# Kernel optimization log

Hardware: AMD Instinct MI355X
Metric: run time of the kernel (lower is better)

## Reference

```python
import jax, jax.numpy as jnp
import numpy as np

N_NODES = 2_000_000
N_EDGES = 16_777_216
N_REL = 4


def setup_inputs() -> dict:
    key = jax.random.key(0)
    ks = jax.random.split(key, 13)
    inp = {
        "author_x": jax.random.normal(ks[0], (N_NODES, 4), jnp.float32),
        "paper_x": jax.random.normal(ks[1], (N_NODES, 4), jnp.float32),
        "src_index": jax.random.randint(ks[2], (N_EDGES,), 0, N_NODES, jnp.int64 if jax.config.jax_enable_x64 else jnp.int32).astype(jnp.int32),
        "dst_index": jax.random.randint(ks[3], (N_EDGES,), 0, N_NODES).astype(jnp.int32),
        "edge_type_index": jax.random.randint(ks[4], (N_EDGES,), 0, N_REL).astype(jnp.int32),
        "edge_src_is_paper": jax.random.randint(ks[5], (N_REL,), 0, 2).astype(jnp.int32),
        "edge_dst_is_paper": jax.random.randint(ks[6], (N_REL,), 0, 2).astype(jnp.int32),
        "Wa": jax.random.normal(ks[7], (4, 4), jnp.float32) * 0.5,
        "ba": jax.random.normal(ks[8], (4,), jnp.float32) * 0.1,
        "Wp": jax.random.normal(ks[9], (4, 4), jnp.float32) * 0.5,
        "bp": jax.random.normal(ks[10], (4,), jnp.float32) * 0.1,
        "Ws": jax.random.normal(ks[11], (8,), jnp.float32) * 0.5,
        "bs": jax.random.normal(ks[12], (1,), jnp.float32) * 0.1,
    }
    return inp


def reference(author_x, paper_x, src_index, dst_index, edge_type_index,
              edge_src_is_paper, edge_dst_is_paper, Wa, ba, Wp, bp, Ws, bs):
    # Encode node tables (tiny GEMMs): [N,4] @ [4,4]^T + [4]
    author_h = author_x @ Wa.T + ba
    paper_h = paper_x @ Wp.T + bp
    # Per-edge relation-type dispatch: 1 = paper table, 0 = author table
    src_p = edge_src_is_paper[edge_type_index].astype(bool)  # [E]
    dst_p = edge_dst_is_paper[edge_type_index].astype(bool)  # [E]
    src_repr = jnp.where(src_p[:, None], paper_h[src_index], author_h[src_index])  # [E,4]
    dst_repr = jnp.where(dst_p[:, None], paper_h[dst_index], author_h[dst_index])  # [E,4]
    # scorer: Linear(8,1) on concat, squeeze last dim -> [E]
    logits = jnp.concatenate([src_repr, dst_repr], axis=-1) @ Ws + bs[0]
    return logits
```

## Files before the change

### kernel.cpp

```cpp
#include <hip/hip_runtime.h>

typedef int         iv4 __attribute__((ext_vector_type(4)));
typedef float       fv4 __attribute__((ext_vector_type(4)));
typedef _Float16    hv4 __attribute__((ext_vector_type(4)));

struct Fold {
    float va_s[4], va_d[4], vp_s[4], vp_d[4];
    float ca_s, ca_d, cp_s, cp_d;
};

__device__ inline Fold make_fold(const float* __restrict__ Wa, const float* __restrict__ ba,
                                 const float* __restrict__ Wp, const float* __restrict__ bp,
                                 const float* __restrict__ Ws) {
    Fold f;
    float w0 = Ws[0], w1 = Ws[1], w2 = Ws[2], w3 = Ws[3];
    float w4 = Ws[4], w5 = Ws[5], w6 = Ws[6], w7 = Ws[7];
#pragma unroll
    for (int j = 0; j < 4; ++j) {
        f.va_s[j] = w0*Wa[j] + w1*Wa[4+j] + w2*Wa[8+j] + w3*Wa[12+j];
        f.va_d[j] = w4*Wa[j] + w5*Wa[4+j] + w6*Wa[8+j] + w7*Wa[12+j];
        f.vp_s[j] = w0*Wp[j] + w1*Wp[4+j] + w2*Wp[8+j] + w3*Wp[12+j];
        f.vp_d[j] = w4*Wp[j] + w5*Wp[4+j] + w6*Wp[8+j] + w7*Wp[12+j];
    }
    f.ca_s = w0*ba[0] + w1*ba[1] + w2*ba[2] + w3*ba[3];
    f.ca_d = w4*ba[0] + w5*ba[1] + w6*ba[2] + w7*ba[3];
    f.cp_s = w0*bp[0] + w1*bp[1] + w2*bp[2] + w3*bp[3];
    f.cp_d = w4*bp[0] + w5*bp[1] + w6*bp[2] + w7*bp[3];
    return f;
}

__device__ inline void node_scores(const Fold& f, fv4 a, fv4 p,
                                   float& as, float& ps, float& ad, float& pd) {
    as = a.x*f.va_s[0] + a.y*f.va_s[1] + a.z*f.va_s[2] + a.w*f.va_s[3] + f.ca_s;
    ad = a.x*f.va_d[0] + a.y*f.va_d[1] + a.z*f.va_d[2] + a.w*f.va_d[3] + f.ca_d;
    ps = p.x*f.vp_s[0] + p.y*f.vp_s[1] + p.z*f.vp_s[2] + p.w*f.vp_s[3] + f.cp_s;
    pd = p.x*f.vp_d[0] + p.y*f.vp_d[1] + p.z*f.vp_d[2] + p.w*f.vp_d[3] + f.cp_d;
}

__global__ __launch_bounds__(256) void node_pass1(
    const fv4* __restrict__ ax, const fv4* __restrict__ px,
    const float* __restrict__ Wa, const float* __restrict__ ba,
    const float* __restrict__ Wp, const float* __restrict__ bp,
    const float* __restrict__ Ws,
    hv4* __restrict__ sc, unsigned* __restrict__ maxes, int n,
    const iv4* __restrict__ et4, unsigned* __restrict__ et8w, int n_et4)
{
    Fold f = make_fold(Wa, ba, Wp, bp, Ws);
    float ms = 0.f, md = 0.f;
    int stride = gridDim.x * blockDim.x;
    int tid0 = blockIdx.x * blockDim.x + threadIdx.x;
    for (int i = tid0; i < n; i += stride) {
        fv4 a = __builtin_nontemporal_load(ax + i);
        fv4 p = __builtin_nontemporal_load(px + i);
        float as, ps, ad, pd;
        node_scores(f, a, p, as, ps, ad, pd);
        hv4 h;
        h.x = (_Float16)as; h.y = (_Float16)ps; h.z = (_Float16)ad; h.w = (_Float16)pd;
        __builtin_nontemporal_store(h, sc + i);
        ms = fmaxf(ms, fmaxf(fabsf(as), fabsf(ps)));
        md = fmaxf(md, fmaxf(fabsf(ad), fabsf(pd)));
    }
    if (et8w) {
        for (int j = tid0; j < n_et4; j += stride) {
            iv4 t = __builtin_nontemporal_load(et4 + j);
            unsigned b = (unsigned)(t.x & 3) | ((unsigned)(t.y & 3) << 8)
                       | ((unsigned)(t.z & 3) << 16) | ((unsigned)(t.w & 3) << 24);
            __builtin_nontemporal_store(b, et8w + j);
        }
    }
#pragma unroll
    for (int off = 32; off >= 1; off >>= 1) {
        ms = fmaxf(ms, __shfl_down(ms, off));
        md = fmaxf(md, __shfl_down(md, off));
    }
    __shared__ float lms[4], lmd[4];
    int wave = threadIdx.x >> 6, lane = threadIdx.x & 63;
    if (lane == 0) { lms[wave] = ms; lmd[wave] = md; }
    __syncthreads();
    if (threadIdx.x == 0) {
        float bms = fmaxf(fmaxf(lms[0], lms[1]), fmaxf(lms[2], lms[3]));
        float bmd = fmaxf(fmaxf(lmd[0], lmd[1]), fmaxf(lmd[2], lmd[3]));
        atomicMax(&maxes[0], __float_as_uint(bms));
        atomicMax(&maxes[1], __float_as_uint(bmd));
    }
}

__global__ __launch_bounds__(256) void node_pass2(
    const hv4* __restrict__ sc, const unsigned* __restrict__ maxes,
    signed char* __restrict__ ts, signed char* __restrict__ td, int n)
{
    int i = blockIdx.x * blockDim.x + threadIdx.x;
    if (i >= n) return;
    float inv_s = 127.f / fmaxf(__uint_as_float(maxes[0]), 1e-20f);
    float inv_d = 127.f / fmaxf(__uint_as_float(maxes[1]), 1e-20f);
    hv4 h = __builtin_nontemporal_load(sc + i);
    int qas = min(127, max(-127, __float2int_rn((float)h.x * inv_s)));
    int qps = min(127, max(-127, __float2int_rn((float)h.y * inv_s)));
    int qad = min(127, max(-127, __float2int_rn((float)h.z * inv_d)));
    int qpd = min(127, max(-127, __float2int_rn((float)h.w * inv_d)));
    ((short*)ts)[i] = (short)(((qps & 0xff) << 8) | (qas & 0xff));
    ((short*)td)[i] = (short)(((qpd & 0xff) << 8) | (qad & 0xff));
}

template<bool E8>
__global__ __launch_bounds__(256) void edge_src_pass(
    const iv4* __restrict__ src4, const iv4* __restrict__ et4,
    const unsigned long long* __restrict__ et8,
    const int* __restrict__ esp,
    const signed char* __restrict__ ts,
    unsigned long long* __restrict__ qsrc, int n8)
{
    int i = blockIdx.x * blockDim.x + threadIdx.x;
    if (i >= n8) return;
    unsigned smask = (unsigned)((esp[0]&1) | ((esp[1]&1)<<1) | ((esp[2]&1)<<2) | ((esp[3]&1)<<3));

    iv4 s0 = __builtin_nontemporal_load(src4 + 2*i);
    iv4 s1 = __builtin_nontemporal_load(src4 + 2*i + 1);
    int ty[8];
    if (E8) {
        unsigned long long tt = __builtin_nontemporal_load(et8 + i);
#pragma unroll
        for (int k = 0; k < 8; ++k) ty[k] = (int)((tt >> (8*k)) & 3ull);
    } else {
        iv4 t0 = __builtin_nontemporal_load(et4 + 2*i);
        iv4 t1 = __builtin_nontemporal_load(et4 + 2*i + 1);
        ty[0]=t0.x&3; ty[1]=t0.y&3; ty[2]=t0.z&3; ty[3]=t0.w&3;
        ty[4]=t1.x&3; ty[5]=t1.y&3; ty[6]=t1.z&3; ty[7]=t1.w&3;
    }
    int sx[8] = { s0.x, s0.y, s0.z, s0.w, s1.x, s1.y, s1.z, s1.w };

    int a[8];
#pragma unroll
    for (int k = 0; k < 8; ++k) a[k] = 2*sx[k] + (int)((smask >> ty[k]) & 1u);

    int q[8];
#pragma unroll
    for (int k = 0; k < 8; ++k) q[k] = (int)ts[a[k]];

    unsigned long long o = 0;
#pragma unroll
    for (int k = 0; k < 8; ++k) o |= (unsigned long long)((unsigned)q[k] & 0xffu) << (8*k);
    __builtin_nontemporal_store(o, qsrc + i);
}

template<bool E8>
__global__ __launch_bounds__(256) void edge_dst_pass(
    const iv4* __restrict__ dst4, const iv4* __restrict__ et4,
    const unsigned long long* __restrict__ et8,
    const int* __restrict__ edp, const float* __restrict__ bs,
    const unsigned* __restrict__ maxes,
    const signed char* __restrict__ td,
    const unsigned long long* __restrict__ qsrc,
    fv4* __restrict__ out4, int n8)
{
    int i = blockIdx.x * blockDim.x + threadIdx.x;
    if (i >= n8) return;
    unsigned dmask = (unsigned)((edp[0]&1) | ((edp[1]&1)<<1) | ((edp[2]&1)<<2) | ((edp[3]&1)<<3));
    float b = bs[0];
    float scale_s = __uint_as_float(maxes[0]) * (1.f / 127.f);
    float scale_d = __uint_as_float(maxes[1]) * (1.f / 127.f);

    iv4 d0 = __builtin_nontemporal_load(dst4 + 2*i);
    iv4 d1 = __builtin_nontemporal_load(dst4 + 2*i + 1);
    int ty[8];
    if (E8) {
        unsigned long long tt = __builtin_nontemporal_load(et8 + i);
#pragma unroll
        for (int k = 0; k < 8; ++k) ty[k] = (int)((tt >> (8*k)) & 3ull);
    } else {
        iv4 t0 = __builtin_nontemporal_load(et4 + 2*i);
        iv4 t1 = __builtin_nontemporal_load(et4 + 2*i + 1);
        ty[0]=t0.x&3; ty[1]=t0.y&3; ty[2]=t0.z&3; ty[3]=t0.w&3;
        ty[4]=t1.x&3; ty[5]=t1.y&3; ty[6]=t1.z&3; ty[7]=t1.w&3;
    }
    unsigned long long qq = __builtin_nontemporal_load(qsrc + i);
    int dx[8] = { d0.x, d0.y, d0.z, d0.w, d1.x, d1.y, d1.z, d1.w };

    int a[8];
#pragma unroll
    for (int k = 0; k < 8; ++k) a[k] = 2*dx[k] + (int)((dmask >> ty[k]) & 1u);

    int qd[8];
#pragma unroll
    for (int k = 0; k < 8; ++k) qd[k] = (int)td[a[k]];

    float r[8];
#pragma unroll
    for (int k = 0; k < 8; ++k) {
        int qs = (int)(signed char)((qq >> (8*k)) & 0xffull);
        r[k] = (float)qs * scale_s + (float)qd[k] * scale_d + b;
    }
    fv4 o0, o1;
    o0.x = r[0]; o0.y = r[1]; o0.z = r[2]; o0.w = r[3];
    o1.x = r[4]; o1.y = r[5]; o1.z = r[6]; o1.w = r[7];
    __builtin_nontemporal_store(o0, out4 + 2*i);
    __builtin_nontemporal_store(o1, out4 + 2*i + 1);
}

__global__ __launch_bounds__(256) void fused_kernel(
    const fv4* __restrict__ ax, const fv4* __restrict__ px,
    const int* __restrict__ src, const int* __restrict__ dst, const int* __restrict__ et,
    const int* __restrict__ esp, const int* __restrict__ edp,
    const float* __restrict__ Wa, const float* __restrict__ ba,
    const float* __restrict__ Wp, const float* __restrict__ bp,
    const float* __restrict__ Ws, const float* __restrict__ bs,
    float* __restrict__ out, int n)
{
    int e = blockIdx.x * blockDim.x + threadIdx.x;
    if (e >= n) return;
    Fold f = make_fold(Wa, ba, Wp, bp, Ws);
    int t = et[e];
    int sp = esp[t] & 1, dp = edp[t] & 1;
    fv4 sv = sp ? px[src[e]] : ax[src[e]];
    fv4 dv = dp ? px[dst[e]] : ax[dst[e]];
    float ssc = sp ? (sv.x*f.vp_s[0] + sv.y*f.vp_s[1] + sv.z*f.vp_s[2] + sv.w*f.vp_s[3] + f.cp_s)
                   : (sv.x*f.va_s[0] + sv.y*f.va_s[1] + sv.z*f.va_s[2] + sv.w*f.va_s[3] + f.ca_s);
    float dsc = dp ? (dv.x*f.vp_d[0] + dv.y*f.vp_d[1] + dv.z*f.vp_d[2] + dv.w*f.vp_d[3] + f.cp_d)
                   : (dv.x*f.va_d[0] + dv.y*f.va_d[1] + dv.z*f.va_d[2] + dv.w*f.va_d[3] + f.ca_d);
    out[e] = ssc + dsc + bs[0];
}

extern "C" void kernel_launch(void* const* d_in, const int* in_sizes, int n_in,
                              void* d_out, int out_size, void* d_ws, size_t ws_size,
                              hipStream_t stream) {
    const float* ax  = (const float*)d_in[0];
    const float* px  = (const float*)d_in[1];
    const int*   src = (const int*)d_in[2];
    const int*   dst = (const int*)d_in[3];
    const int*   et  = (const int*)d_in[4];
    const int*   esp = (const int*)d_in[5];
    const int*   edp = (const int*)d_in[6];
    const float* Wa  = (const float*)d_in[7];
    const float* ba  = (const float*)d_in[8];
    const float* Wp  = (const float*)d_in[9];
    const float* bp  = (const float*)d_in[10];
    const float* Ws  = (const float*)d_in[11];
    const float* bs  = (const float*)d_in[12];
    float* out = (float*)d_out;

    const int n_nodes = in_sizes[0] / 4;
    const int n_edges = in_sizes[2];

    auto rnd = [](size_t v) { return (v + 255) & ~(size_t)255; };
    size_t union_sz = rnd((size_t)n_edges > (size_t)n_nodes * 8 ? (size_t)n_edges
                                                                : (size_t)n_nodes * 8);
    const size_t off_u   = 256;
    const size_t off_ts  = off_u + union_sz;
    const size_t off_td  = off_ts + rnd((size_t)n_nodes * 2);
    const size_t off_e8  = off_td + rnd((size_t)n_nodes * 2);
    const size_t need    = off_e8;
    const size_t need_e8 = off_e8 + rnd((size_t)n_edges);

    if (ws_size >= need && (n_edges & 7) == 0) {
        const bool use_e8 = (ws_size >= need_e8);
        unsigned* maxes = (unsigned*)d_ws;
        hv4* sc = (hv4*)((char*)d_ws + off_u);
        unsigned long long* qsrc = (unsigned long long*)((char*)d_ws + off_u);
        signed char* ts = (signed char*)((char*)d_ws + off_ts);
        signed char* td = (signed char*)((char*)d_ws + off_td);
        unsigned* et8w = use_e8 ? (unsigned*)((char*)d_ws + off_e8) : nullptr;
        const unsigned long long* et8 = (const unsigned long long*)((char*)d_ws + off_e8);

        (void)hipMemsetAsync(maxes, 0, 2 * sizeof(unsigned), stream);
        node_pass1<<<2048, 256, 0, stream>>>(
            (const fv4*)ax, (const fv4*)px, Wa, ba, Wp, bp, Ws, sc, maxes, n_nodes,
            (const iv4*)et, et8w, n_edges / 4);
        node_pass2<<<(n_nodes + 255) / 256, 256, 0, stream>>>(
            sc, maxes, ts, td, n_nodes);

        const int n8 = n_edges / 8;
        const int nb = (n8 + 255) / 256;
        if (use_e8) {
            edge_src_pass<true><<<nb, 256, 0, stream>>>(
                (const iv4*)src, (const iv4*)et, et8, esp, ts, qsrc, n8);
            edge_dst_pass<true><<<nb, 256, 0, stream>>>(
                (const iv4*)dst, (const iv4*)et, et8, edp, bs, maxes, td, qsrc,
                (fv4*)out, n8);
        } else {
            edge_src_pass<false><<<nb, 256, 0, stream>>>(
                (const iv4*)src, (const iv4*)et, et8, esp, ts, qsrc, n8);
            edge_dst_pass<false><<<nb, 256, 0, stream>>>(
                (const iv4*)dst, (const iv4*)et, et8, edp, bs, maxes, td, qsrc,
                (fv4*)out, n8);
        }
    } else {
        fused_kernel<<<(n_edges + 255) / 256, 256, 0, stream>>>(
            (const fv4*)ax, (const fv4*)px, src, dst, et, esp, edp,
            Wa, ba, Wp, bp, Ws, bs, out, n_edges);
    }
}
```

Measured before the change: 456.9 us.

## Replace packed edge-type pass with per-edge dst-table bits from src pass

Edge types are no longer repacked into bytes inside node_pass1. The source pass now reads the full int32 edge types once and writes one byte of destination-table bits per 8 edges, which the destination pass reads instead of the edge types. node_pass2 now handles four nodes per thread with 64-bit packed stores, and cached stores replace nontemporal ones for the intermediates. This cuts edge-type traffic to a single full read plus a small bitmask, but adds a requirement that the node count be divisible by four.

```diff
diff --git a/kernel.cpp b/kernel.cpp
--- a/kernel.cpp
+++ b/kernel.cpp
@@ -42,31 +42,21 @@
     const float* __restrict__ Wa, const float* __restrict__ ba,
     const float* __restrict__ Wp, const float* __restrict__ bp,
     const float* __restrict__ Ws,
-    hv4* __restrict__ sc, unsigned* __restrict__ maxes, int n,
-    const iv4* __restrict__ et4, unsigned* __restrict__ et8w, int n_et4)
+    hv4* __restrict__ sc, unsigned* __restrict__ maxes, int n)
 {
     Fold f = make_fold(Wa, ba, Wp, bp, Ws);
     float ms = 0.f, md = 0.f;
     int stride = gridDim.x * blockDim.x;
-    int tid0 = blockIdx.x * blockDim.x + threadIdx.x;
-    for (int i = tid0; i < n; i += stride) {
+    for (int i = blockIdx.x * blockDim.x + threadIdx.x; i < n; i += stride) {
         fv4 a = __builtin_nontemporal_load(ax + i);
         fv4 p = __builtin_nontemporal_load(px + i);
         float as, ps, ad, pd;
         node_scores(f, a, p, as, ps, ad, pd);
         hv4 h;
         h.x = (_Float16)as; h.y = (_Float16)ps; h.z = (_Float16)ad; h.w = (_Float16)pd;
-        __builtin_nontemporal_store(h, sc + i);
+        sc[i] = h;
         ms = fmaxf(ms, fmaxf(fabsf(as), fabsf(ps)));
         md = fmaxf(md, fmaxf(fabsf(ad), fabsf(pd)));
-    }
-    if (et8w) {
-        for (int j = tid0; j < n_et4; j += stride) {
-            iv4 t = __builtin_nontemporal_load(et4 + j);
-            unsigned b = (unsigned)(t.x & 3) | ((unsigned)(t.y & 3) << 8)
-                       | ((unsigned)(t.z & 3) << 16) | ((unsigned)(t.w & 3) << 24);
-            __builtin_nontemporal_store(b, et8w + j);
-        }
     }
 #pragma unroll
     for (int off = 32; off >= 1; off >>= 1) {
@@ -87,46 +77,46 @@
 
 __global__ __launch_bounds__(256) void node_pass2(
     const hv4* __restrict__ sc, const unsigned* __restrict__ maxes,
-    signed char* __restrict__ ts, signed char* __restrict__ td, int n)
+    unsigned long long* __restrict__ ts8, unsigned long long* __restrict__ td8, int n4)
 {
     int i = blockIdx.x * blockDim.x + threadIdx.x;
-    if (i >= n) return;
+    if (i >= n4) return;
     float inv_s = 127.f / fmaxf(__uint_as_float(maxes[0]), 1e-20f);
     float inv_d = 127.f / fmaxf(__uint_as_float(maxes[1]), 1e-20f);
-    hv4 h = __builtin_nontemporal_load(sc + i);
-    int qas = min(127, max(-127, __float2int_rn((float)h.x * inv_s)));
-    int qps = min(127, max(-127, __float2int_rn((float)h.y * inv_s)));
-    int qad = min(127, max(-127, __float2int_rn((float)h.z * inv_d)));
-    int qpd = min(127, max(-127, __float2int_rn((float)h.w * inv_d)));
-    ((short*)ts)[i] = (short)(((qps & 0xff) << 8) | (qas & 0xff));
-    ((short*)td)[i] = (short)(((qpd & 0xff) << 8) | (qad & 0xff));
-}
-
-template<bool E8>
+    unsigned long long vs = 0, vd = 0;
+#pragma unroll
+    for (int j = 0; j < 4; ++j) {
+        hv4 h = sc[4*i + j];
+        int qas = min(127, max(-127, __float2int_rn((float)h.x * inv_s)));
+        int qps = min(127, max(-127, __float2int_rn((float)h.y * inv_s)));
+        int qad = min(127, max(-127, __float2int_rn((float)h.z * inv_d)));
+        int qpd = min(127, max(-127, __float2int_rn((float)h.w * inv_d)));
+        vs |= (unsigned long long)((unsigned)qas & 0xffu) << (16*j);
+        vs |= (unsigned long long)((unsigned)qps & 0xffu) << (16*j + 8);
+        vd |= (unsigned long long)((unsigned)qad & 0xffu) << (16*j);
+        vd |= (unsigned long long)((unsigned)qpd & 0xffu) << (16*j + 8);
+    }
+    ts8[i] = vs;
+    td8[i] = vd;
+}
+
 __global__ __launch_bounds__(256) void edge_src_pass(
     const iv4* __restrict__ src4, const iv4* __restrict__ et4,
-    const unsigned long long* __restrict__ et8,
-    const int* __restrict__ esp,
+    const int* __restrict__ esp, const int* __restrict__ edp,
     const signed char* __restrict__ ts,
-    unsigned long long* __restrict__ qsrc, int n8)
+    unsigned long long* __restrict__ qsrc,
+    unsigned char* __restrict__ dbits, int n8)
 {
     int i = blockIdx.x * blockDim.x + threadIdx.x;
     if (i >= n8) return;
     unsigned smask = (unsigned)((esp[0]&1) | ((esp[1]&1)<<1) | ((esp[2]&1)<<2) | ((esp[3]&1)<<3));
+    unsigned dmask = (unsigned)((edp[0]&1) | ((edp[1]&1)<<1) | ((edp[2]&1)<<2) | ((edp[3]&1)<<3));
 
     iv4 s0 = __builtin_nontemporal_load(src4 + 2*i);
     iv4 s1 = __builtin_nontemporal_load(src4 + 2*i + 1);
-    int ty[8];
-    if (E8) {
-        unsigned long long tt = __builtin_nontemporal_load(et8 + i);
-#pragma unroll
-        for (int k = 0; k < 8; ++k) ty[k] = (int)((tt >> (8*k)) & 3ull);
-    } else {
-        iv4 t0 = __builtin_nontemporal_load(et4 + 2*i);
-        iv4 t1 = __builtin_nontemporal_load(et4 + 2*i + 1);
-        ty[0]=t0.x&3; ty[1]=t0.y&3; ty[2]=t0.z&3; ty[3]=t0.w&3;
-        ty[4]=t1.x&3; ty[5]=t1.y&3; ty[6]=t1.z&3; ty[7]=t1.w&3;
-    }
+    iv4 t0 = __builtin_nontemporal_load(et4 + 2*i);
+    iv4 t1 = __builtin_nontemporal_load(et4 + 2*i + 1);
+    int ty[8] = { t0.x&3, t0.y&3, t0.z&3, t0.w&3, t1.x&3, t1.y&3, t1.z&3, t1.w&3 };
     int sx[8] = { s0.x, s0.y, s0.z, s0.w, s1.x, s1.y, s1.z, s1.w };
 
     int a[8];
@@ -138,47 +128,39 @@
     for (int k = 0; k < 8; ++k) q[k] = (int)ts[a[k]];
 
     unsigned long long o = 0;
-#pragma unroll
-    for (int k = 0; k < 8; ++k) o |= (unsigned long long)((unsigned)q[k] & 0xffu) << (8*k);
+    unsigned db = 0;
+#pragma unroll
+    for (int k = 0; k < 8; ++k) {
+        o |= (unsigned long long)((unsigned)q[k] & 0xffu) << (8*k);
+        db |= ((dmask >> ty[k]) & 1u) << k;
+    }
     __builtin_nontemporal_store(o, qsrc + i);
-}
-
-template<bool E8>
+    __builtin_nontemporal_store((unsigned char)db, dbits + i);
+}
+
 __global__ __launch_bounds__(256) void edge_dst_pass(
-    const iv4* __restrict__ dst4, const iv4* __restrict__ et4,
-    const unsigned long long* __restrict__ et8,
-    const int* __restrict__ edp, const float* __restrict__ bs,
-    const unsigned* __restrict__ maxes,
+    const iv4* __restrict__ dst4,
+    const unsigned char* __restrict__ dbits,
+    const float* __restrict__ bs, const unsigned* __restrict__ maxes,
     const signed char* __restrict__ td,
     const unsigned long long* __restrict__ qsrc,
     fv4* __restrict__ out4, int n8)
 {
     int i = blockIdx.x * blockDim.x + threadIdx.x;
     if (i >= n8) return;
-    unsigned dmask = (unsigned)((edp[0]&1) | ((edp[1]&1)<<1) | ((edp[2]&1)<<2) | ((edp[3]&1)<<3));
     float b = bs[0];
     float scale_s = __uint_as_float(maxes[0]) * (1.f / 127.f);
     float scale_d = __uint_as_float(maxes[1]) * (1.f / 127.f);
 
     iv4 d0 = __builtin_nontemporal_load(dst4 + 2*i);
     iv4 d1 = __builtin_nontemporal_load(dst4 + 2*i + 1);
-    int ty[8];
-    if (E8) {
-        unsigned long long tt = __builtin_nontemporal_load(et8 + i);
-#pragma unroll
-        for (int k = 0; k < 8; ++k) ty[k] = (int)((tt >> (8*k)) & 3ull);
-    } else {
-        iv4 t0 = __builtin_nontemporal_load(et4 + 2*i);
-        iv4 t1 = __builtin_nontemporal_load(et4 + 2*i + 1);
-        ty[0]=t0.x&3; ty[1]=t0.y&3; ty[2]=t0.z&3; ty[3]=t0.w&3;
-        ty[4]=t1.x&3; ty[5]=t1.y&3; ty[6]=t1.z&3; ty[7]=t1.w&3;
-    }
-    unsigned long long qq = __builtin_nontemporal_load(qsrc + i);
+    unsigned db = (unsigned)dbits[i];
+    unsigned long long qq = qsrc[i];
     int dx[8] = { d0.x, d0.y, d0.z, d0.w, d1.x, d1.y, d1.z, d1.w };
 
     int a[8];
 #pragma unroll
-    for (int k = 0; k < 8; ++k) a[k] = 2*dx[k] + (int)((dmask >> ty[k]) & 1u);
+    for (int k = 0; k < 8; ++k) a[k] = 2*dx[k] + (int)((db >> k) & 1u);
 
     int qd[8];
 #pragma unroll
@@ -244,45 +226,33 @@
     auto rnd = [](size_t v) { return (v + 255) & ~(size_t)255; };
     size_t union_sz = rnd((size_t)n_edges > (size_t)n_nodes * 8 ? (size_t)n_edges
                                                                 : (size_t)n_nodes * 8);
-    const size_t off_u   = 256;
-    const size_t off_ts  = off_u + union_sz;
-    const size_t off_td  = off_ts + rnd((size_t)n_nodes * 2);
-    const size_t off_e8  = off_td + rnd((size_t)n_nodes * 2);
-    const size_t need    = off_e8;
-    const size_t need_e8 = off_e8 + rnd((size_t)n_edges);
-
-    if (ws_size >= need && (n_edges & 7) == 0) {
-        const bool use_e8 = (ws_size >= need_e8);
+    const size_t off_u  = 256;
+    const size_t off_ts = off_u + union_sz;
+    const size_t off_td = off_ts + rnd((size_t)n_nodes * 2);
+    const size_t off_db = off_td + rnd((size_t)n_nodes * 2);
+    const size_t need   = off_db + rnd((size_t)(n_edges / 8) + 1);
+
+    if (ws_size >= need && (n_edges & 7) == 0 && (n_nodes & 3) == 0) {
         unsigned* maxes = (unsigned*)d_ws;
         hv4* sc = (hv4*)((char*)d_ws + off_u);
         unsigned long long* qsrc = (unsigned long long*)((char*)d_ws + off_u);
         signed char* ts = (signed char*)((char*)d_ws + off_ts);
         signed char* td = (signed char*)((char*)d_ws + off_td);
-        unsigned* et8w = use_e8 ? (unsigned*)((char*)d_ws + off_e8) : nullptr;
-        const unsigned long long* et8 = (const unsigned long long*)((char*)d_ws + off_e8);
+        unsigned char* dbits = (unsigned char*)((char*)d_ws + off_db);
 
         (void)hipMemsetAsync(maxes, 0, 2 * sizeof(unsigned), stream);
         node_pass1<<<2048, 256, 0, stream>>>(
-            (const fv4*)ax, (const fv4*)px, Wa, ba, Wp, bp, Ws, sc, maxes, n_nodes,
-            (const iv4*)et, et8w, n_edges / 4);
-        node_pass2<<<(n_nodes + 255) / 256, 256, 0, stream>>>(
-            sc, maxes, ts, td, n_nodes);
+            (const fv4*)ax, (const fv4*)px, Wa, ba, Wp, bp, Ws, sc, maxes, n_nodes);
+        const int n4 = n_nodes / 4;
+        node_pass2<<<(n4 + 255) / 256, 256, 0, stream>>>(
+            sc, maxes, (unsigned long long*)ts, (unsigned long long*)td, n4);
 
         const int n8 = n_edges / 8;
         const int nb = (n8 + 255) / 256;
-        if (use_e8) {
-            edge_src_pass<true><<<nb, 256, 0, stream>>>(
-                (const iv4*)src, (const iv4*)et, et8, esp, ts, qsrc, n8);
-            edge_dst_pass<true><<<nb, 256, 0, stream>>>(
-                (const iv4*)dst, (const iv4*)et, et8, edp, bs, maxes, td, qsrc,
-                (fv4*)out, n8);
-        } else {
-            edge_src_pass<false><<<nb, 256, 0, stream>>>(
-                (const iv4*)src, (const iv4*)et, et8, esp, ts, qsrc, n8);
-            edge_dst_pass<false><<<nb, 256, 0, stream>>>(
-                (const iv4*)dst, (const iv4*)et, et8, edp, bs, maxes, td, qsrc,
-                (fv4*)out, n8);
-        }
+        edge_src_pass<<<nb, 256, 0, stream>>>(
+            (const iv4*)src, (const iv4*)et, esp, edp, ts, qsrc, dbits, n8);
+        edge_dst_pass<<<nb, 256, 0, stream>>>(
+            (const iv4*)dst, dbits, bs, maxes, td, qsrc, (fv4*)out, n8);
     } else {
         fused_kernel<<<(n_edges + 255) / 256, 256, 0, stream>>>(
             (const fv4*)ax, (const fv4*)px, src, dst, et, esp, edp,
```

Result: no change. 460.1 us (+0.7%).
